# Performance work log

Measured on AMD Instinct MI355X. Metric: run time of the kernel, lower is better.

Reference implementation:

```python
import jax, jax.numpy as jnp
import numpy as np

B, T, F, H = 256, 1024, 64, 128
DT = 1.0
EPS = 1e-5


def _layer_norm(h, g, b):
    mu = jnp.mean(h, axis=-1, keepdims=True)
    var = jnp.var(h, axis=-1, keepdims=True)
    return (h - mu) * jax.lax.rsqrt(var + EPS) * g + b


def setup_inputs() -> dict:
    key = jax.random.key(0)
    ks = jax.random.split(key, 8)
    def xavier(k, shape):
        fan_in, fan_out = shape[1], shape[0]
        lim = np.sqrt(6.0 / (fan_in + fan_out))
        return jax.random.uniform(k, shape, jnp.float32, -lim, lim)
    return {
        "x": jax.random.normal(ks[0], (B, T, F), jnp.float32),
        # layer 0 (input_dim=F)
        "Wh0": xavier(ks[1], (H, H)), "bh0": jnp.zeros((H,), jnp.float32),
        "Wx0": xavier(ks[2], (H, F)), "bx0": jnp.zeros((H,), jnp.float32),
        "Wt0": xavier(ks[3], (H, F)), "bt0": jnp.zeros((H,), jnp.float32),
        "tau0": jnp.ones((H,), jnp.float32),
        "g0": jnp.ones((H,), jnp.float32), "be0": jnp.zeros((H,), jnp.float32),
        # layer 1 (input_dim=H)
        "Wh1": xavier(ks[4], (H, H)), "bh1": jnp.zeros((H,), jnp.float32),
        "Wx1": xavier(ks[5], (H, H)), "bx1": jnp.zeros((H,), jnp.float32),
        "Wt1": xavier(ks[6], (H, H)), "bt1": jnp.zeros((H,), jnp.float32),
        "tau1": jnp.ones((H,), jnp.float32),
        "g1": jnp.ones((H,), jnp.float32), "be1": jnp.zeros((H,), jnp.float32),
    }


def _cell(x_t, h, Wh, bh, Wx, bx, Wt, bt, tau_base):
    f = jnp.tanh(h @ Wh.T + bh + x_t @ Wx.T + bx)        # (B,H)
    tau = tau_base + jax.nn.softplus(x_t @ Wt.T + bt)     # (B,H)
    return h + (DT / tau) * (-h + f)


def reference(x, Wh0, bh0, Wx0, bx0, Wt0, bt0, tau0, g0, be0,
              Wh1, bh1, Wx1, bx1, Wt1, bt1, tau1, g1, be1):
    xT = jnp.transpose(x, (1, 0, 2))  # (T,B,F)

    def step(carry, x_t):
        h0, h1 = carry
        h0 = _layer_norm(_cell(x_t, h0, Wh0, bh0, Wx0, bx0, Wt0, bt0, tau0), g0, be0)
        h1 = _layer_norm(_cell(h0, h1, Wh1, bh1, Wx1, bx1, Wt1, bt1, tau1), g1, be1)
        return (h0, h1), None

    h_init = (jnp.zeros((x.shape[0], H), x.dtype), jnp.zeros((x.shape[0], H), x.dtype))
    (h0, h1), _ = jax.lax.scan(step, h_init, xT)
    return h1  # hidden_dim == latent_dim, no proj
```

## Files before the change

kernel.cpp:

```cpp
#include <hip/hip_runtime.h>
#include <stdint.h>


#define B_ 256
#define T_ 1024
#define F_ 64
#define H_ 128
#define EPS_ 1e-5f
#define NT_ 512

typedef _Float16 h2 __attribute__((ext_vector_type(2)));
typedef _Float16 h8 __attribute__((ext_vector_type(8)));
typedef float f32x4 __attribute__((ext_vector_type(4)));
typedef __fp16  f16v2 __attribute__((ext_vector_type(2)));

__device__ __forceinline__ h2 pkf16(float a, float b) {
  union { f16v2 f; h2 h; } c;
  c.f = __builtin_amdgcn_cvt_pkrtz(a, b);
  return c.h;
}
__device__ __forceinline__ uint32_t as_u32(h2 h) { union { h2 h; uint32_t u; } c; c.h = h; return c.u; }

__device__ __forceinline__ void wg_barrier() {
  asm volatile("s_waitcnt lgkmcnt(0)\n\ts_barrier" ::: "memory");
}

#if __has_builtin(__builtin_amdgcn_rsqf)
__device__ __forceinline__ float rsq_fast(float x) { return __builtin_amdgcn_rsqf(x); }
#else
__device__ __forceinline__ float rsq_fast(float x) { return rsqrtf(x); }
#endif

#if __has_builtin(__builtin_amdgcn_update_dpp)
template <int CTRL>
__device__ __forceinline__ float dpp_add(float v) {
  union { float f; int i; } a, b;
  a.f = v;
  b.i = __builtin_amdgcn_update_dpp(0, a.i, CTRL, 0xf, 0xf, true);
  return v + b.f;
}
__device__ __forceinline__ float red16(float v) {
  v = dpp_add<0x128>(v);
  v = dpp_add<0x124>(v);
  v = dpp_add<0x122>(v);
  v = dpp_add<0x121>(v);
  return v;
}
#else
__device__ __forceinline__ float red16(float v) {
  v += __shfl_xor(v, 1); v += __shfl_xor(v, 2);
  v += __shfl_xor(v, 4); v += __shfl_xor(v, 8);
  return v;
}
#endif

__device__ __forceinline__ h8 packfrag(const float* p) {
  float4 a = *(const float4*)p;
  float4 b = *(const float4*)(p + 4);
  union { h2 h[4]; h8 v; } c;
  c.h[0] = pkf16(a.x, a.y); c.h[1] = pkf16(a.z, a.w);
  c.h[2] = pkf16(b.x, b.y); c.h[3] = pkf16(b.z, b.w);
  return c.v;
}
__device__ __forceinline__ h8 packfrag_g(const float* w, const float* gv, const float* bv,
                                         float& dg, float& dbe) {
  float4 a = *(const float4*)w;
  float4 b = *(const float4*)(w + 4);
  float4 ga = *(const float4*)gv;
  float4 gb = *(const float4*)(gv + 4);
  float4 ba = *(const float4*)bv;
  float4 bb = *(const float4*)(bv + 4);
  float w0 = a.x*ga.x, w1 = a.y*ga.y, w2 = a.z*ga.z, w3 = a.w*ga.w;
  float w4 = b.x*gb.x, w5 = b.y*gb.y, w6 = b.z*gb.z, w7 = b.w*gb.w;
  dg  += (w0 + w1) + (w2 + w3) + (w4 + w5) + (w6 + w7);
  dbe += a.x*ba.x + a.y*ba.y + a.z*ba.z + a.w*ba.w
       + b.x*bb.x + b.y*bb.y + b.z*bb.z + b.w*bb.w;
  union { h2 h[4]; h8 v; } c;
  c.h[0] = pkf16(w0, w1); c.h[1] = pkf16(w2, w3);
  c.h[2] = pkf16(w4, w5); c.h[3] = pkf16(w6, w7);
  return c.v;
}
__device__ __forceinline__ h8 ldfrag(const uint32_t* p) {
  union { uint4 u; h8 v; } c;
  c.u = *(const uint4*)p;
  return c.v;
}

__device__ __forceinline__ float tanh_fast(float a) {
  float aa = fabsf(a);
  float e  = __expf(2.f * aa);
  float th = 1.f - 2.f * __builtin_amdgcn_rcpf(e + 1.f);
  return copysignf(th, a);
}
__device__ __forceinline__ float softplus_fast(float x) {
  return (x > 20.f) ? x : __logf(1.f + __expf(x));
}

#define MFMA16(A_, B_, C_) __builtin_amdgcn_mfma_f32_16x16x32_f16(A_, B_, C_, 0, 0, 0)

__global__ void __attribute__((amdgpu_flat_work_group_size(NT_, NT_)))
                __attribute__((amdgpu_waves_per_eu(2, 2)))
ltc_scan(
    const float* __restrict__ x,
    const float* __restrict__ Wh0, const float* __restrict__ bh0,
    const float* __restrict__ Wx0, const float* __restrict__ bx0,
    const float* __restrict__ Wt0, const float* __restrict__ bt0,
    const float* __restrict__ tau0, const float* __restrict__ g0,
    const float* __restrict__ be0,
    const float* __restrict__ Wh1, const float* __restrict__ bh1,
    const float* __restrict__ Wx1, const float* __restrict__ bx1,
    const float* __restrict__ Wt1, const float* __restrict__ bt1,
    const float* __restrict__ tau1, const float* __restrict__ g1,
    const float* __restrict__ be1,
    float* __restrict__ out)
{
  __shared__ __align__(16) uint32_t h0p[2][64];
  __shared__ __align__(16) uint32_t h1p[2][64];
  __shared__ __align__(16) uint32_t hn0p[4][64];
  __shared__ __align__(16) uint32_t x4[4][32];
  __shared__ __align__(16) float2   p0s[4][4];
  __shared__ __align__(16) float2   p1s[4][4];

  const int tid = threadIdx.x;
  const int wid = tid >> 6;
  const int l   = tid & 63;
  const int g4  = (l >> 4) << 2;
  const int g8  = (l >> 4) << 3;
  const int b   = blockIdx.x;
  const float* xg = x + (size_t)b * (T_ * F_);
  const bool selT1 = (l & 16) != 0;

  if (tid < 128) { ((uint32_t*)h0p)[tid] = 0u; ((uint32_t*)h1p)[tid] = 0u; }
  if (tid < 32)  { ((float*)p0s)[tid] = 0.f; ((float*)p1s)[tid] = 0.f; }
  if (tid < 32) {
    float2 a = *(const float2*)(xg + 2 * tid);
    float2 c = *(const float2*)(xg + F_ + 2 * tid);
    x4[0][tid] = as_u32(pkf16(a.x, a.y));
    x4[1][tid] = as_u32(pkf16(c.x, c.y));
  }
  __syncthreads();

  if (wid < 4) {
    const int c0 = wid * 32 + (l & 15);
    const int ct = wid * 32 + (l & 31);
    h8 wh0[4], wh1[4], wx0[2], wx1[2], wt0[2], wt1[2];
    float cg, cb;
    {
      float dg0 = 0.f, db0 = 0.f, dg1 = 0.f, db1 = 0.f;
      const float* p0 = Wh0 + c0 * H_ + g8;
      const float* p1 = Wh0 + (c0 + 16) * H_ + g8;
      #pragma unroll
      for (int m = 0; m < 4; ++m) {
        wh0[m] = packfrag_g(p0 + 32 * m, g0 + g8 + 32 * m, be0 + g8 + 32 * m, dg0, db0);
        wh1[m] = packfrag_g(p1 + 32 * m, g0 + g8 + 32 * m, be0 + g8 + 32 * m, dg1, db1);
      }
      dg0 += __shfl_xor(dg0, 16); dg0 += __shfl_xor(dg0, 32);
      db0 += __shfl_xor(db0, 16); db0 += __shfl_xor(db0, 32);
      dg1 += __shfl_xor(dg1, 16); dg1 += __shfl_xor(dg1, 32);
      db1 += __shfl_xor(db1, 16); db1 += __shfl_xor(db1, 32);
      cg = selT1 ? dg1 : dg0; cb = selT1 ? db1 : db0;
      const float* q0 = Wx0 + c0 * F_ + g8;
      const float* q1 = Wx0 + (c0 + 16) * F_ + g8;
      const float* r0 = Wt0 + c0 * F_ + g8;
      const float* r1 = Wt0 + (c0 + 16) * F_ + g8;
      #pragma unroll
      for (int m = 0; m < 2; ++m) {
        wx0[m] = packfrag(q0 + 32 * m); wx1[m] = packfrag(q1 + 32 * m);
        wt0[m] = packfrag(r0 + 32 * m); wt1[m] = packfrag(r1 + 32 * m);
      }
    }
    const float bhx = bh0[ct] + bx0[ct];
    const float btr = bt0[ct], taub = tau0[ct], gr = g0[ct], ber = be0[ct];
    const int  widx = wid * 16 + ((l & 31) >> 1);
    const bool wlane = ((l & 33) == 0);
    const bool st = (wid == 0) && (l < 32);

    float hcp = 0.f;
    float2 xc0, xc1;
    if (st) {
      xc0 = *(const float2*)(xg + 2 * F_ + 2 * l);
      xc1 = *(const float2*)(xg + 3 * F_ + 2 * l);
    }
    float xcs, tcs;
    {
      const uint32_t* xb = x4[0];
      f32x4 nX0 = {0.f,0.f,0.f,0.f}, nX1 = {0.f,0.f,0.f,0.f};
      f32x4 nT0 = {0.f,0.f,0.f,0.f}, nT1 = {0.f,0.f,0.f,0.f};
      #pragma unroll
      for (int m = 0; m < 2; ++m) {
        h8 xf = ldfrag(xb + m * 16 + g4);
        nX0 = MFMA16(xf, wx0[m], nX0);
        nX1 = MFMA16(xf, wx1[m], nX1);
        nT0 = MFMA16(xf, wt0[m], nT0);
        nT1 = MFMA16(xf, wt1[m], nT1);
      }
      xcs = (selT1 ? nX1[0] : nX0[0]) + bhx;
      tcs = (selT1 ? nT1[0] : nT0[0]) + btr;
    }

    #pragma unroll 4
    for (int p = 0; p <= T_ + 1; ++p) {
      if (p <= T_) {
        const int i = p;
        const float4* sp = (const float4*)&p0s[(i + 3) & 3][0];
        float4 sa = sp[0], sb = sp[1];
        float ss  = (sa.x + sa.z) + (sb.x + sb.z);
        float s2s = (sa.y + sa.w) + (sb.y + sb.w);
        if (st) {
          x4[(i + 2) & 3][l] = as_u32(pkf16(xc0.x, xc0.y));
          xc0 = xc1;
          int tn = (i + 4 < T_) ? (i + 4) : (T_ - 1);
          xc1 = *(const float2*)(xg + tn * F_ + 2 * l);
        }
        const uint32_t* ub = h0p[(i + 1) & 1];
        f32x4 aH0a = {0.f,0.f,0.f,0.f}, aH0b = {0.f,0.f,0.f,0.f};
        f32x4 aH1a = {0.f,0.f,0.f,0.f}, aH1b = {0.f,0.f,0.f,0.f};
        {
          h8 af0 = ldfrag(ub + g4);
          h8 af1 = ldfrag(ub + 16 + g4);
          h8 af2 = ldfrag(ub + 32 + g4);
          h8 af3 = ldfrag(ub + 48 + g4);
          aH0a = MFMA16(af0, wh0[0], aH0a); aH1a = MFMA16(af0, wh1[0], aH1a);
          aH0b = MFMA16(af1, wh0[1], aH0b); aH1b = MFMA16(af1, wh1[1], aH1b);
          aH0a = MFMA16(af2, wh0[2], aH0a); aH1a = MFMA16(af2, wh1[2], aH1a);
          aH0b = MFMA16(af3, wh0[3], aH0b); aH1b = MFMA16(af3, wh1[3], aH1b);
        }
        float aH = selT1 ? (aH1a[0] + aH1b[0]) : (aH0a[0] + aH0b[0]);
        float mu = ss * (1.f / 128.f);
        float m2 = s2s * (1.f / 128.f);
        float rstd = rsq_fast(m2 - mu * mu + EPS_);
        float fl = (i > 0) ? 1.f : 0.f;
        float sc = fl * rstd;
        float pa = fmaf(sc, aH, fmaf(-sc * mu, cg, fl * cb)) + xcs;
        float pt = tcs;
        float f   = tanh_fast(pa);
        float tau = taub + softplus_fast(pt);
        float hold = fl * fmaf((hcp - mu) * rstd, gr, ber);
        float hc  = fmaf(f - hold, __builtin_amdgcn_rcpf(tau), hold);
        float hn2 = __shfl_xor(hold, 1);
        if (wlane) hn0p[(i + 3) & 3][widx] = as_u32(pkf16(hold, hn2));
        float hc2 = __shfl_xor(hc, 1);
        if (wlane) h0p[i & 1][widx] = as_u32(pkf16(hc, hc2));
        float v = (l & 32) ? hc * hc : hc;
        v = red16(v); v += __shfl_xor(v, 16);
        float v2 = __shfl_down(v, 32);
        if (l == 0) p0s[i & 3][wid] = make_float2(v, v2);
        hcp = hc;
        {
          const uint32_t* xb = x4[(i + 1) & 3];
          f32x4 nX0 = {0.f,0.f,0.f,0.f}, nX1 = {0.f,0.f,0.f,0.f};
          f32x4 nT0 = {0.f,0.f,0.f,0.f}, nT1 = {0.f,0.f,0.f,0.f};
          #pragma unroll
          for (int m = 0; m < 2; ++m) {
            h8 xf = ldfrag(xb + m * 16 + g4);
            nX0 = MFMA16(xf, wx0[m], nX0);
            nX1 = MFMA16(xf, wx1[m], nX1);
            nT0 = MFMA16(xf, wt0[m], nT0);
            nT1 = MFMA16(xf, wt1[m], nT1);
          }
          xcs = (selT1 ? nX1[0] : nX0[0]) + bhx;
          tcs = (selT1 ? nT1[0] : nT0[0]) + btr;
        }
      }
      wg_barrier();
    }
  } else {
    const int c0 = (wid - 4) * 32 + (l & 15);
    const int ct = (wid - 4) * 32 + (l & 31);
    h8 vh0[4], vh1[4], vx0[4], vx1[4], vt0[4], vt1[4];
    float cAg, cAb;
    {
      float d1 = 0.f, d2 = 0.f, e1 = 0.f, e2 = 0.f;
      const float* p0 = Wh1 + c0 * H_ + g8;
      const float* p1 = Wh1 + (c0 + 16) * H_ + g8;
      const float* q0 = Wx1 + c0 * H_ + g8;
      const float* q1 = Wx1 + (c0 + 16) * H_ + g8;
      const float* r0 = Wt1 + c0 * H_ + g8;
      const float* r1 = Wt1 + (c0 + 16) * H_ + g8;
      #pragma unroll
      for (int m = 0; m < 4; ++m) {
        vh0[m] = packfrag_g(p0 + 32 * m, g1 + g8 + 32 * m, be1 + g8 + 32 * m, d1, d2);
        vh1[m] = packfrag_g(p1 + 32 * m, g1 + g8 + 32 * m, be1 + g8 + 32 * m, e1, e2);
        vx0[m] = packfrag(q0 + 32 * m); vx1[m] = packfrag(q1 + 32 * m);
        vt0[m] = packfrag(r0 + 32 * m); vt1[m] = packfrag(r1 + 32 * m);
      }
      d1 += __shfl_xor(d1, 16); d1 += __shfl_xor(d1, 32);
      d2 += __shfl_xor(d2, 16); d2 += __shfl_xor(d2, 32);
      e1 += __shfl_xor(e1, 16); e1 += __shfl_xor(e1, 32);
      e2 += __shfl_xor(e2, 16); e2 += __shfl_xor(e2, 32);
      cAg = selT1 ? e1 : d1; cAb = selT1 ? e2 : d2;
    }
    const float bhx = bh1[ct] + bx1[ct];
    const float btr = bt1[ct], taub = tau1[ct], gr = g1[ct], ber = be1[ct];
    const int  widx = (wid - 4) * 16 + ((l & 31) >> 1);
    const bool wlane = ((l & 33) == 0);
    const int  bw = wid - 4;

    float hcp = 0.f;
    #pragma unroll 2
    for (int p = 0; p <= T_ + 1; ++p) {
      if (p >= 2) {
        const int j = p - 2;
        const float4* sp = (const float4*)&p1s[(j + 3) & 3][0];
        float4 sa = sp[0], sb = sp[1];
        float ss1 = (sa.x + sa.z) + (sb.x + sb.z);
        float s21 = (sa.y + sa.w) + (sb.y + sb.w);
        const uint32_t* u1b = h1p[(j + 1) & 1];
        const uint32_t* hnb = hn0p[j & 3];
        f32x4 aA0 = {0.f,0.f,0.f,0.f}, aA1 = {0.f,0.f,0.f,0.f};
        f32x4 aB0 = {0.f,0.f,0.f,0.f}, aB1 = {0.f,0.f,0.f,0.f};
        f32x4 aT0 = {0.f,0.f,0.f,0.f}, aT1 = {0.f,0.f,0.f,0.f};
        #pragma unroll
        for (int m = 0; m < 4; ++m) {
          h8 af = ldfrag(u1b + m * 16 + g4);
          aA0 = MFMA16(af, vh0[m], aA0);
          aA1 = MFMA16(af, vh1[m], aA1);
        }
        #pragma unroll
        for (int m = 0; m < 4; ++m) {
          h8 f0 = ldfrag(hnb + m * 16 + g4);
          aB0 = MFMA16(f0, vx0[m], aB0);
          aB1 = MFMA16(f0, vx1[m], aB1);
          aT0 = MFMA16(f0, vt0[m], aT0);
          aT1 = MFMA16(f0, vt1[m], aT1);
        }
        float aA = selT1 ? aA1[0] : aA0[0];
        float aB = selT1 ? aB1[0] : aB0[0];
        float aT = selT1 ? aT1[0] : aT0[0];
        float mu1 = ss1 * (1.f / 128.f);
        float m21 = s21 * (1.f / 128.f);
        float rstd1 = rsq_fast(m21 - mu1 * mu1 + EPS_);
        float fl1 = (j > 0) ? 1.f : 0.f;
        float sc1 = fl1 * rstd1;
        float pa = fmaf(sc1, aA, fmaf(-sc1 * mu1, cAg, fl1 * cAb)) + aB + bhx;
        float pt = aT + btr;
        float f   = tanh_fast(pa);
        float tau = taub + softplus_fast(pt);
        float hold = fl1 * fmaf((hcp - mu1) * rstd1, gr, ber);
        float hc  = fmaf(f - hold, __builtin_amdgcn_rcpf(tau), hold);
        float hc2 = __shfl_xor(hc, 1);
        if (wlane) h1p[j & 1][widx] = as_u32(pkf16(hc, hc2));
        float v = (l & 32) ? hc * hc : hc;
        v = red16(v); v += __shfl_xor(v, 16);
        float v2 = __shfl_down(v, 32);
        if (l == 0) p1s[j & 3][bw] = make_float2(v, v2);
        hcp = hc;
      }
      wg_barrier();
    }
    {
      const float4* sp = (const float4*)&p1s[(T_ - 1) & 3][0];
      float4 sa = sp[0], sb = sp[1];
      float ss1 = (sa.x + sa.z) + (sb.x + sb.z);
      float s21 = (sa.y + sa.w) + (sb.y + sb.w);
      float mu1 = ss1 * (1.f / 128.f);
      float m21 = s21 * (1.f / 128.f);
      float rstd1 = rsq_fast(m21 - mu1 * mu1 + EPS_);
      float hn = fmaf((hcp - mu1) * rstd1, gr, ber);
      if (l < 32) out[b * H_ + ct] = hn;
    }
  }
}

extern "C" void kernel_launch(void* const* d_in, const int* in_sizes, int n_in,
                              void* d_out, int out_size, void* d_ws, size_t ws_size,
                              hipStream_t stream) {
  const float* x    = (const float*)d_in[0];
  const float* Wh0  = (const float*)d_in[1];
  const float* bh0  = (const float*)d_in[2];
  const float* Wx0  = (const float*)d_in[3];
  const float* bx0  = (const float*)d_in[4];
  const float* Wt0  = (const float*)d_in[5];
  const float* bt0  = (const float*)d_in[6];
  const float* tau0 = (const float*)d_in[7];
  const float* g0   = (const float*)d_in[8];
  const float* be0  = (const float*)d_in[9];
  const float* Wh1  = (const float*)d_in[10];
  const float* bh1  = (const float*)d_in[11];
  const float* Wx1  = (const float*)d_in[12];
  const float* bx1  = (const float*)d_in[13];
  const float* Wt1  = (const float*)d_in[14];
  const float* bt1  = (const float*)d_in[15];
  const float* tau1 = (const float*)d_in[16];
  const float* g1   = (const float*)d_in[17];
  const float* be1  = (const float*)d_in[18];
  float* out        = (float*)d_out;

  ltc_scan<<<B_, NT_, 0, stream>>>(x, Wh0, bh0, Wx0, bx0, Wt0, bt0, tau0, g0, be0,
                                   Wh1, bh1, Wx1, bx1, Wt1, bt1, tau1, g1, be1, out);
}
```

Baseline: 834.5 us.

## Software-pipeline layer-1 input projections one step ahead of the recurrence

The layer-1 waves now compute the Wx/Wt projections of the layer-0 output for step j+1 in the same iteration as the recurrent update for step j. This takes those 16 MFMAs off the serial dependency chain and adds one extra pipeline stage to both loops. The recurrent Wh MFMAs are also split across two accumulator chains with all fragments loaded up front, to shorten MFMA dependency latency. The cost is one extra barrier iteration and more live registers, and it depends on the hn0p ring buffer being deep enough for the added lag.

Measured after the change: 846.3 us. Within noise of the previous version (+1.4%).

```diff
diff --git a/kernel.cpp b/kernel.cpp
--- a/kernel.cpp
+++ b/kernel.cpp
@@ -199,7 +199,7 @@
     }
 
     #pragma unroll 4
-    for (int p = 0; p <= T_ + 1; ++p) {
+    for (int p = 0; p <= T_ + 2; ++p) {
       if (p <= T_) {
         const int i = p;
         const float4* sp = (const float4*)&p0s[(i + 3) & 3][0];
@@ -297,43 +297,36 @@
     const int  bw = wid - 4;
 
     float hcp = 0.f;
+    float bcs = 0.f, tcs = 0.f;
     #pragma unroll 2
-    for (int p = 0; p <= T_ + 1; ++p) {
-      if (p >= 2) {
-        const int j = p - 2;
+    for (int p = 0; p <= T_ + 2; ++p) {
+      if (p >= 3) {
+        const int j = p - 3;
         const float4* sp = (const float4*)&p1s[(j + 3) & 3][0];
         float4 sa = sp[0], sb = sp[1];
         float ss1 = (sa.x + sa.z) + (sb.x + sb.z);
         float s21 = (sa.y + sa.w) + (sb.y + sb.w);
         const uint32_t* u1b = h1p[(j + 1) & 1];
-        const uint32_t* hnb = hn0p[j & 3];
-        f32x4 aA0 = {0.f,0.f,0.f,0.f}, aA1 = {0.f,0.f,0.f,0.f};
-        f32x4 aB0 = {0.f,0.f,0.f,0.f}, aB1 = {0.f,0.f,0.f,0.f};
-        f32x4 aT0 = {0.f,0.f,0.f,0.f}, aT1 = {0.f,0.f,0.f,0.f};
-        #pragma unroll
-        for (int m = 0; m < 4; ++m) {
-          h8 af = ldfrag(u1b + m * 16 + g4);
-          aA0 = MFMA16(af, vh0[m], aA0);
-          aA1 = MFMA16(af, vh1[m], aA1);
-        }
-        #pragma unroll
-        for (int m = 0; m < 4; ++m) {
-          h8 f0 = ldfrag(hnb + m * 16 + g4);
-          aB0 = MFMA16(f0, vx0[m], aB0);
-          aB1 = MFMA16(f0, vx1[m], aB1);
-          aT0 = MFMA16(f0, vt0[m], aT0);
-          aT1 = MFMA16(f0, vt1[m], aT1);
-        }
-        float aA = selT1 ? aA1[0] : aA0[0];
-        float aB = selT1 ? aB1[0] : aB0[0];
-        float aT = selT1 ? aT1[0] : aT0[0];
+        f32x4 aA0a = {0.f,0.f,0.f,0.f}, aA0b = {0.f,0.f,0.f,0.f};
+        f32x4 aA1a = {0.f,0.f,0.f,0.f}, aA1b = {0.f,0.f,0.f,0.f};
+        {
+          h8 af0 = ldfrag(u1b + g4);
+          h8 af1 = ldfrag(u1b + 16 + g4);
+          h8 af2 = ldfrag(u1b + 32 + g4);
+          h8 af3 = ldfrag(u1b + 48 + g4);
+          aA0a = MFMA16(af0, vh0[0], aA0a); aA1a = MFMA16(af0, vh1[0], aA1a);
+          aA0b = MFMA16(af1, vh0[1], aA0b); aA1b = MFMA16(af1, vh1[1], aA1b);
+          aA0a = MFMA16(af2, vh0[2], aA0a); aA1a = MFMA16(af2, vh1[2], aA1a);
+          aA0b = MFMA16(af3, vh0[3], aA0b); aA1b = MFMA16(af3, vh1[3], aA1b);
+        }
+        float aA = selT1 ? (aA1a[0] + aA1b[0]) : (aA0a[0] + aA0b[0]);
         float mu1 = ss1 * (1.f / 128.f);
         float m21 = s21 * (1.f / 128.f);
         float rstd1 = rsq_fast(m21 - mu1 * mu1 + EPS_);
         float fl1 = (j > 0) ? 1.f : 0.f;
         float sc1 = fl1 * rstd1;
-        float pa = fmaf(sc1, aA, fmaf(-sc1 * mu1, cAg, fl1 * cAb)) + aB + bhx;
-        float pt = aT + btr;
+        float pa = fmaf(sc1, aA, fmaf(-sc1 * mu1, cAg, fl1 * cAb)) + bcs;
+        float pt = tcs;
         float f   = tanh_fast(pa);
         float tau = taub + softplus_fast(pt);
         float hold = fl1 * fmaf((hcp - mu1) * rstd1, gr, ber);
@@ -345,6 +338,21 @@
         float v2 = __shfl_down(v, 32);
         if (l == 0) p1s[j & 3][bw] = make_float2(v, v2);
         hcp = hc;
+      }
+      if (p >= 2 && p <= T_ + 1) {
+        const uint32_t* hnb = hn0p[(p - 2) & 3];
+        f32x4 nB0 = {0.f,0.f,0.f,0.f}, nB1 = {0.f,0.f,0.f,0.f};
+        f32x4 nT0 = {0.f,0.f,0.f,0.f}, nT1 = {0.f,0.f,0.f,0.f};
+        #pragma unroll
+        for (int m = 0; m < 4; ++m) {
+          h8 f0 = ldfrag(hnb + m * 16 + g4);
+          nB0 = MFMA16(f0, vx0[m], nB0);
+          nB1 = MFMA16(f0, vx1[m], nB1);
+          nT0 = MFMA16(f0, vt0[m], nT0);
+          nT1 = MFMA16(f0, vt1[m], nT1);
+        }
+        bcs = (selT1 ? nB1[0] : nB0[0]) + bhx;
+        tcs = (selT1 ? nT1[0] : nT0[0]) + btr;
       }
       wg_barrier();
     }
```
